# Optimization experiments

Hardware: AMD Instinct MI355X
Metric: run time of the kernel (lower is better)

The kernel has to match this reference:

```python
import jax, jax.numpy as jnp
import numpy as np

N_NODES = 100000
N_EDGES = 3200000
IN_DIM = 512
HEADS = 4
C1 = 8   # conv1 per-head channels
C2 = 4   # conv2 per-head channels
OUT_DIM = 10
N_GRAPHS = 64
NEG_SLOPE = 0.2


def _leaky_relu(x):
    return jnp.where(x >= 0, x, NEG_SLOPE * x)


def gat_conv(x, src, dst, W, a_src, a_dst, b):
    """PyG GATConv (concat=True). x:[N,F], src/dst:[E], W:[F,H*C], a_*:[H,C], b:[H*C]."""
    N = x.shape[0]
    H, C = a_src.shape
    h = (x @ W).reshape(N, H, C)                      # [N,H,C]
    e_src = jnp.einsum('nhc,hc->nh', h, a_src)        # [N,H]
    e_dst = jnp.einsum('nhc,hc->nh', h, a_dst)
    e = _leaky_relu(e_src[src] + e_dst[dst])          # [E,H]
    # segment softmax over edges grouped by destination node
    m = jax.ops.segment_max(e, dst, num_segments=N)   # [N,H]
    ex = jnp.exp(e - m[dst])
    denom = jax.ops.segment_sum(ex, dst, num_segments=N)
    alpha = ex / (denom[dst] + 1e-16)                 # [E,H]
    out = jax.ops.segment_sum(h[src] * alpha[:, :, None], dst, num_segments=N)
    return out.reshape(N, H * C) + b


def setup_inputs() -> dict:
    key = jax.random.key(0)
    ks = jax.random.split(key, 16)
    x = jax.random.normal(ks[0], (N_NODES, IN_DIM), dtype=jnp.float32)
    edge_index = jax.random.randint(ks[1], (2, N_EDGES), 0, N_NODES, dtype=jnp.int64)
    batch = jnp.sort(jax.random.randint(ks[2], (N_NODES,), 0, N_GRAPHS, dtype=jnp.int64))
    def glorot(k, shape):
        fan_in = shape[0] if len(shape) == 2 else shape[-1]
        return jax.random.normal(k, shape, dtype=jnp.float32) * (1.0 / np.sqrt(fan_in))
    return {
        'x': x, 'edge_index': edge_index, 'batch': batch,
        'W1': glorot(ks[3], (IN_DIM, HEADS * C1)),
        'att_src1': glorot(ks[4], (HEADS, C1)),
        'att_dst1': glorot(ks[5], (HEADS, C1)),
        'b1': jnp.zeros((HEADS * C1,), jnp.float32),
        'W2': glorot(ks[6], (HEADS * C1, HEADS * C2)),
        'att_src2': glorot(ks[7], (HEADS, C2)),
        'att_dst2': glorot(ks[8], (HEADS, C2)),
        'b2': jnp.zeros((HEADS * C2,), jnp.float32),
        'Wf': glorot(ks[9], (HEADS * C2, OUT_DIM)),
        'bf': jnp.zeros((OUT_DIM,), jnp.float32),
    }


def reference(x, edge_index, batch, W1, att_src1, att_dst1, b1,
              W2, att_src2, att_dst2, b2, Wf, bf):
    N = x.shape[0]
    loops = jnp.arange(N, dtype=edge_index.dtype)     # add_self_loops=True
    src = jnp.concatenate([edge_index[0], loops])
    dst = jnp.concatenate([edge_index[1], loops])
    h = jax.nn.relu(gat_conv(x, src, dst, W1, att_src1, att_dst1, b1))
    h = jax.nn.relu(gat_conv(h, src, dst, W2, att_src2, att_dst2, b2))
    # global_mean_pool over graphs
    sums = jax.ops.segment_sum(h, batch, num_segments=N_GRAPHS)
    cnt = jax.ops.segment_sum(jnp.ones((N,), h.dtype), batch, num_segments=N_GRAPHS)
    pooled = sums / jnp.maximum(cnt, 1.0)[:, None]    # [G, 16]
    return pooled @ Wf + bf
```

## Files before the change

### kernel.cpp

```cpp
#include <hip/hip_runtime.h>


#define LRELU(v) ((v) >= 0.f ? (v) : 0.2f * (v))

__global__ __launch_bounds__(256) void k_bin(const int* __restrict__ ei,
                                             int2* __restrict__ stg,
                                             int* __restrict__ rcnt,
                                             int E0, int Etot, int nr, int cap) {
    __shared__ int cnt[1024];
    __shared__ int base[1024];
    const int t = threadIdx.x;
    for (int i = t; i < nr; i += 256) cnt[i] = 0;
    __syncthreads();
    const int e0 = blockIdx.x * 8192;
#pragma unroll 4
    for (int k = 0; k < 32; k++) {
        int e = e0 + k * 256 + t;
        if (e < Etot) {
            int d = (e < E0) ? ei[E0 + e] : (e - E0);
            atomicAdd(&cnt[d >> 8], 1);
        }
    }
    __syncthreads();
    for (int i = t; i < nr; i += 256) {
        int c = cnt[i];
        base[i] = c ? atomicAdd(&rcnt[i], c) : 0;
        cnt[i] = 0;
    }
    __syncthreads();
#pragma unroll 4
    for (int k = 0; k < 32; k++) {
        int e = e0 + k * 256 + t;
        if (e < Etot) {
            int s, d;
            if (e < E0) {
                s = ei[e];
                d = ei[E0 + e];
            } else {
                s = d = e - E0;
            }
            int r = d >> 8;
            int slot = base[r] + atomicAdd(&cnt[r], 1);
            stg[(size_t)r * cap + slot] = make_int2(s, d);
        }
    }
}

__global__ __launch_bounds__(512) void k_sort(const int2* __restrict__ stg,
                                              const int* __restrict__ rcnt,
                                              int* __restrict__ row_ptr,
                                              int* __restrict__ ssrc,
                                              int* __restrict__ sdst,
                                              int N, int Etot, int nr, int cap) {
    __shared__ int hist[256];
    __shared__ int hs[256];
    __shared__ int red[512];
    const int r = blockIdx.x;
    const int t = threadIdx.x;
    int part = 0;
    for (int i = t; i < r; i += 512) part += rcnt[i];
    red[t] = part;
    if (t < 256) hist[t] = 0;
    __syncthreads();
    for (int off = 256; off > 0; off >>= 1) {
        if (t < off) red[t] += red[t + off];
        __syncthreads();
    }
    const int rb = red[0];
    const int n0 = r << 8;
    const int cnt = rcnt[r];
    const int2* seg = stg + (size_t)r * cap;
    for (int i = t; i < cnt; i += 512) {
        int d = seg[i].y;
        atomicAdd(&hist[d - n0], 1);
    }
    __syncthreads();
    if (t < 256) hs[t] = hist[t];
    __syncthreads();
    for (int off = 1; off < 256; off <<= 1) {
        int o = (t < 256 && t >= off) ? hs[t - off] : 0;
        __syncthreads();
        if (t < 256) hs[t] += o;
        __syncthreads();
    }
    if (t < 256) {
        int excl = hs[t] - hist[t];
        int node = n0 + t;
        if (node < N) row_ptr[node] = rb + excl;
        hist[t] = excl;
    }
    if (r == nr - 1 && t == 0) row_ptr[N] = Etot;
    __syncthreads();
    for (int i = t; i < cnt; i += 512) {
        int2 sd2 = seg[i];
        int off = atomicAdd(&hist[sd2.y - n0], 1);
        ssrc[rb + off] = sd2.x;
        sdst[rb + off] = sd2.y;
    }
}

__global__ __launch_bounds__(256) void k_gemm1(const float* __restrict__ x,
                                               const float* __restrict__ W,
                                               const float* __restrict__ a_src,
                                               const float* __restrict__ a_dst,
                                               float* __restrict__ h,
                                               float* __restrict__ es,
                                               float* __restrict__ ed, int N) {
    __shared__ float xs[32 * 132];
    __shared__ float ws[32 * 36];
    const int t = threadIdx.x;
    const int r0 = (t >> 2) * 2;
    const int cg = t & 3;
    const int row0 = blockIdx.x * 128;

    float acc[2][8];
#pragma unroll
    for (int i = 0; i < 2; i++)
#pragma unroll
        for (int j = 0; j < 8; j++) acc[i][j] = 0.f;

    float4 xr[4];
    float4 wr;
    const int xrow = t >> 3, xc4 = t & 7;
    const int wk = t >> 3, wc4 = t & 7;

    auto load_chunk = [&](int kc) {
#pragma unroll
        for (int ii = 0; ii < 4; ii++) {
            int row = xrow + ii * 32;
            int rr = row0 + row;
            if (rr >= N) rr = N - 1;
            xr[ii] = *(const float4*)&x[(size_t)rr * 512 + kc + xc4 * 4];
        }
        wr = *(const float4*)&W[(size_t)(kc + wk) * 32 + wc4 * 4];
    };

    load_chunk(0);
    for (int c = 0; c < 16; c++) {
        __syncthreads();
#pragma unroll
        for (int ii = 0; ii < 4; ii++) {
            int row = xrow + ii * 32;
            xs[(xc4 * 4 + 0) * 132 + row] = xr[ii].x;
            xs[(xc4 * 4 + 1) * 132 + row] = xr[ii].y;
            xs[(xc4 * 4 + 2) * 132 + row] = xr[ii].z;
            xs[(xc4 * 4 + 3) * 132 + row] = xr[ii].w;
        }
        ws[wk * 36 + wc4 * 4 + 0] = wr.x;
        ws[wk * 36 + wc4 * 4 + 1] = wr.y;
        ws[wk * 36 + wc4 * 4 + 2] = wr.z;
        ws[wk * 36 + wc4 * 4 + 3] = wr.w;
        __syncthreads();
        if (c < 15) load_chunk((c + 1) * 32);
#pragma unroll 8
        for (int k = 0; k < 32; k++) {
            float2 xv = *(const float2*)&xs[k * 132 + r0];
            float4 w0 = *(const float4*)&ws[k * 36 + cg * 8];
            float4 w1 = *(const float4*)&ws[k * 36 + cg * 8 + 4];
            acc[0][0] += xv.x * w0.x;
            acc[0][1] += xv.x * w0.y;
            acc[0][2] += xv.x * w0.z;
            acc[0][3] += xv.x * w0.w;
            acc[0][4] += xv.x * w1.x;
            acc[0][5] += xv.x * w1.y;
            acc[0][6] += xv.x * w1.z;
            acc[0][7] += xv.x * w1.w;
            acc[1][0] += xv.y * w0.x;
            acc[1][1] += xv.y * w0.y;
            acc[1][2] += xv.y * w0.z;
            acc[1][3] += xv.y * w0.w;
            acc[1][4] += xv.y * w1.x;
            acc[1][5] += xv.y * w1.y;
            acc[1][6] += xv.y * w1.z;
            acc[1][7] += xv.y * w1.w;
        }
    }

    float4 as0 = *(const float4*)&a_src[cg * 8];
    float4 as1 = *(const float4*)&a_src[cg * 8 + 4];
    float4 ad0 = *(const float4*)&a_dst[cg * 8];
    float4 ad1 = *(const float4*)&a_dst[cg * 8 + 4];
#pragma unroll
    for (int i = 0; i < 2; i++) {
        int r = row0 + r0 + i;
        if (r < N) {
            *(float4*)&h[(size_t)r * 32 + cg * 8] =
                make_float4(acc[i][0], acc[i][1], acc[i][2], acc[i][3]);
            *(float4*)&h[(size_t)r * 32 + cg * 8 + 4] =
                make_float4(acc[i][4], acc[i][5], acc[i][6], acc[i][7]);
            es[r * 4 + cg] = acc[i][0] * as0.x + acc[i][1] * as0.y +
                             acc[i][2] * as0.z + acc[i][3] * as0.w +
                             acc[i][4] * as1.x + acc[i][5] * as1.y +
                             acc[i][6] * as1.z + acc[i][7] * as1.w;
            ed[r * 4 + cg] = acc[i][0] * ad0.x + acc[i][1] * ad0.y +
                             acc[i][2] * ad0.z + acc[i][3] * ad0.w +
                             acc[i][4] * ad1.x + acc[i][5] * ad1.y +
                             acc[i][6] * ad1.z + acc[i][7] * ad1.w;
        }
    }
}

__global__ __launch_bounds__(256) void k_alpha(const int* __restrict__ ssrc,
                                               const int* __restrict__ sdst,
                                               const float* __restrict__ es,
                                               const float* __restrict__ ed,
                                               float4* __restrict__ alf, int Etot) {
    int i = blockIdx.x * 256 + threadIdx.x;
    if (i >= Etot) return;
    int s = ssrc[i];
    int d = sdst[i];
    float4 a = *(const float4*)&es[(size_t)s * 4];
    float4 b = *(const float4*)&ed[(size_t)d * 4];
    float4 o;
    float v;
    v = a.x + b.x; o.x = __expf(LRELU(v));
    v = a.y + b.y; o.y = __expf(LRELU(v));
    v = a.z + b.z; o.z = __expf(LRELU(v));
    v = a.w + b.w; o.w = __expf(LRELU(v));
    alf[i] = o;
}

template <int HC>
__global__ __launch_bounds__(256) void k_agg(const int* __restrict__ row_ptr,
                                             const int* __restrict__ ssrc,
                                             const float* __restrict__ hsrc,
                                             const float4* __restrict__ alf,
                                             const float* __restrict__ bias,
                                             float* __restrict__ out, int N) {
    constexpr int E2 = 64 / HC;
    constexpr int U = 8;
    const int lane = threadIdx.x & 63;
    const int d = blockIdx.x * 4 + (threadIdx.x >> 6);
    if (d >= N) return;
    const int c = lane & (HC - 1);
    const int e2 = lane / HC;
    const int hh = c / (HC / 4);
    const int start = row_ptr[d];
    const int deg = row_ptr[d + 1] - start;
    const int j0 = (e2 < deg) ? e2 : 0;

    float l = 0.f, acc = 0.f;
    for (int jb = e2; jb < deg; jb += U * E2) {
        int idx[U];
        float wv[U];
#pragma unroll
        for (int u = 0; u < U; u++) {
            int jj = jb + u * E2;
            bool ok = jj < deg;
            wv[u] = ok ? 1.f : 0.f;
            idx[u] = start + (ok ? jj : j0);
        }
        int sv[U];
#pragma unroll
        for (int u = 0; u < U; u++) sv[u] = ssrc[idx[u]];
        float av[U];
#pragma unroll
        for (int u = 0; u < U; u++)
            av[u] = ((const float*)&alf[idx[u]])[hh] * wv[u];
        float hv[U];
#pragma unroll
        for (int u = 0; u < U; u++) hv[u] = hsrc[(size_t)sv[u] * HC + c];
#pragma unroll
        for (int u = 0; u < U; u++) {
            l += av[u];
            acc += av[u] * hv[u];
        }
    }
#pragma unroll
    for (int off = HC; off < 64; off <<= 1) {
        l += __shfl_xor(l, off);
        acc += __shfl_xor(acc, off);
    }
    if (lane < HC) {
        float v = acc / (l + 1e-16f) + bias[c];
        out[(size_t)d * HC + c] = v > 0.f ? v : 0.f;
    }
}

__global__ __launch_bounds__(256) void k_gemm2(const float* __restrict__ g1,
                                               const float* __restrict__ W2,
                                               const float* __restrict__ a2s,
                                               const float* __restrict__ a2d,
                                               float* __restrict__ h2,
                                               float* __restrict__ es2,
                                               float* __restrict__ ed2, int N) {
    __shared__ float rows[64 * 33];
    __shared__ float ws[32 * 20];
    int t = threadIdx.x;
    int n0 = blockIdx.x * 64;
#pragma unroll
    for (int ii = 0; ii < 2; ii++) {
        int idx = ii * 256 + t;
        int node = idx >> 3, c4 = idx & 7;
        float4 v = make_float4(0.f, 0.f, 0.f, 0.f);
        if (n0 + node < N) v = *(const float4*)&g1[(size_t)(n0 + node) * 32 + c4 * 4];
        rows[node * 33 + c4 * 4 + 0] = v.x;
        rows[node * 33 + c4 * 4 + 1] = v.y;
        rows[node * 33 + c4 * 4 + 2] = v.z;
        rows[node * 33 + c4 * 4 + 3] = v.w;
    }
    if (t < 128) {
        int r = t >> 2, c4 = t & 3;
        float4 v = *(const float4*)&W2[r * 16 + c4 * 4];
        ws[r * 20 + c4 * 4 + 0] = v.x;
        ws[r * 20 + c4 * 4 + 1] = v.y;
        ws[r * 20 + c4 * 4 + 2] = v.z;
        ws[r * 20 + c4 * 4 + 3] = v.w;
    }
    __syncthreads();
    int node = t >> 2, q = t & 3;
    int n = n0 + node;
    if (n >= N) return;
    float acc[4] = {0.f, 0.f, 0.f, 0.f};
#pragma unroll 8
    for (int cc = 0; cc < 32; cc++) {
        float v = rows[node * 33 + cc];
        float4 w = *(const float4*)&ws[cc * 20 + q * 4];
        acc[0] += v * w.x;
        acc[1] += v * w.y;
        acc[2] += v * w.z;
        acc[3] += v * w.w;
    }
    *(float4*)&h2[(size_t)n * 16 + q * 4] = make_float4(acc[0], acc[1], acc[2], acc[3]);
    float s1 = 0.f, s2 = 0.f;
#pragma unroll
    for (int j = 0; j < 4; j++) {
        s1 += acc[j] * a2s[q * 4 + j];
        s2 += acc[j] * a2d[q * 4 + j];
    }
    es2[n * 4 + q] = s1;
    ed2[n * 4 + q] = s2;
}

__global__ __launch_bounds__(256) void k_final(const float* __restrict__ h3,
                                               const int* __restrict__ batch,
                                               const float* __restrict__ Wf,
                                               const float* __restrict__ bf,
                                               float* __restrict__ out, int N) {
    __shared__ float part[16][17];
    __shared__ float pooled[16];
    int g = blockIdx.x;
    int t = threadIdx.x;

    int lo = 0, b = N;
    while (lo < b) { int mid = (lo + b) >> 1; if (batch[mid] < g) lo = mid + 1; else b = mid; }
    int hi = lo; b = N;
    while (hi < b) { int mid = (hi + b) >> 1; if (batch[mid] < g + 1) hi = mid + 1; else b = mid; }

    int ch = t & 15, r = t >> 4;
    float acc = 0.f;
    for (int i = lo + r; i < hi; i += 16) acc += h3[(size_t)i * 16 + ch];
    part[r][ch] = acc;
    __syncthreads();
    if (t < 16) {
        float s = 0.f;
#pragma unroll
        for (int rr = 0; rr < 16; rr++) s += part[rr][t];
        float cnt = (float)(hi - lo);
        pooled[t] = s / fmaxf(cnt, 1.f);
    }
    __syncthreads();
    if (t < 10) {
        float v = bf[t];
#pragma unroll
        for (int cc = 0; cc < 16; cc++) v += pooled[cc] * Wf[cc * 10 + t];
        out[g * 10 + t] = v;
    }
}

extern "C" void kernel_launch(void* const* d_in, const int* in_sizes, int n_in,
                              void* d_out, int out_size, void* d_ws, size_t ws_size,
                              hipStream_t stream) {
    const float* x   = (const float*)d_in[0];
    const int*   ei  = (const int*)d_in[1];
    const int*   bat = (const int*)d_in[2];
    const float* W1  = (const float*)d_in[3];
    const float* as1 = (const float*)d_in[4];
    const float* ad1 = (const float*)d_in[5];
    const float* b1  = (const float*)d_in[6];
    const float* W2  = (const float*)d_in[7];
    const float* as2 = (const float*)d_in[8];
    const float* ad2 = (const float*)d_in[9];
    const float* b2  = (const float*)d_in[10];
    const float* Wf  = (const float*)d_in[11];
    const float* bf  = (const float*)d_in[12];
    float* outp = (float*)d_out;

    const int N = in_sizes[2];
    const int E0 = in_sizes[1] / 2;
    const int Etot = E0 + N;
    const int nr = (N + 255) >> 8;
    const int cap = Etot / nr + 2048;

    char* w = (char*)d_ws;
    auto alloc = [&](size_t bytes) -> char* {
        char* p = w;
        w += (bytes + 255) & ~(size_t)255;
        return p;
    };
    float* h1  = (float*)alloc((size_t)N * 32 * 4);
    float* es1 = (float*)alloc((size_t)N * 4 * 4);
    float* ed1 = (float*)alloc((size_t)N * 4 * 4);
    float* g1  = (float*)alloc((size_t)N * 32 * 4);
    float* h2  = (float*)alloc((size_t)N * 16 * 4);
    float* es2 = (float*)alloc((size_t)N * 4 * 4);
    float* ed2 = (float*)alloc((size_t)N * 4 * 4);
    int* rcnt    = (int*)alloc(4096);
    int* row_ptr = (int*)alloc((size_t)(N + 1) * 4);
    int* ssrc    = (int*)alloc((size_t)Etot * 4);
    int* sdst    = (int*)alloc((size_t)Etot * 4);
    float4* alf  = (float4*)alloc((size_t)Etot * 16);
    int2* stg    = (int2*)alloc((size_t)nr * cap * 8);
    float* h3 = h1;

    const int nb1 = (N + 127) / 128;
    const int nbe = (Etot + 255) / 256;

    hipMemsetAsync(rcnt, 0, 4096, stream);
    k_bin<<<(Etot + 8191) / 8192, 256, 0, stream>>>(ei, stg, rcnt, E0, Etot, nr, cap);
    k_sort<<<nr, 512, 0, stream>>>(stg, rcnt, row_ptr, ssrc, sdst, N, Etot, nr, cap);
    k_gemm1<<<nb1, 256, 0, stream>>>(x, W1, as1, ad1, h1, es1, ed1, N);
    k_alpha<<<nbe, 256, 0, stream>>>(ssrc, sdst, es1, ed1, alf, Etot);
    k_agg<32><<<(N + 3) / 4, 256, 0, stream>>>(row_ptr, ssrc, h1, alf, b1, g1, N);
    k_gemm2<<<(N + 63) / 64, 256, 0, stream>>>(g1, W2, as2, ad2, h2, es2, ed2, N);
    k_alpha<<<nbe, 256, 0, stream>>>(ssrc, sdst, es2, ed2, alf, Etot);
    k_agg<16><<<(N + 3) / 4, 256, 0, stream>>>(row_ptr, ssrc, h2, alf, b2, h3, N);
    k_final<<<64, 256, 0, stream>>>(h3, bat, Wf, bf, outp, N);
}
```

Measured before the change: 660.4 us.

## Fuse edge attention computation into aggregation kernels and drop sdst/alpha buffers

Removes the separate per-edge alpha kernels and computes exp(leaky_relu(es[src]+ed[dst])) inline inside the CSR aggregation, since the destination is fixed per wavefront. This drops the sdst array write in the sort and the 16-byte-per-edge alpha buffer round trip through memory. The aggregation is also restructured to use float4 feature loads per lane, with more edges processed in parallel per wave, and an adjusted unroll. In exchange, exp is recomputed per channel group, and the es gather adds a dependent load after the source index lookup.

```diff
diff --git a/kernel.cpp b/kernel.cpp
--- a/kernel.cpp
+++ b/kernel.cpp
@@ -50,7 +50,6 @@
                                               const int* __restrict__ rcnt,
                                               int* __restrict__ row_ptr,
                                               int* __restrict__ ssrc,
-                                              int* __restrict__ sdst,
                                               int N, int Etot, int nr, int cap) {
     __shared__ int hist[256];
     __shared__ int hs[256];
@@ -95,7 +94,6 @@
         int2 sd2 = seg[i];
         int off = atomicAdd(&hist[sd2.y - n0], 1);
         ssrc[rb + off] = sd2.x;
-        sdst[rb + off] = sd2.y;
     }
 }
 
@@ -200,52 +198,33 @@
     }
 }
 
-__global__ __launch_bounds__(256) void k_alpha(const int* __restrict__ ssrc,
-                                               const int* __restrict__ sdst,
-                                               const float* __restrict__ es,
-                                               const float* __restrict__ ed,
-                                               float4* __restrict__ alf, int Etot) {
-    int i = blockIdx.x * 256 + threadIdx.x;
-    if (i >= Etot) return;
-    int s = ssrc[i];
-    int d = sdst[i];
-    float4 a = *(const float4*)&es[(size_t)s * 4];
-    float4 b = *(const float4*)&ed[(size_t)d * 4];
-    float4 o;
-    float v;
-    v = a.x + b.x; o.x = __expf(LRELU(v));
-    v = a.y + b.y; o.y = __expf(LRELU(v));
-    v = a.z + b.z; o.z = __expf(LRELU(v));
-    v = a.w + b.w; o.w = __expf(LRELU(v));
-    alf[i] = o;
-}
-
-template <int HC>
-__global__ __launch_bounds__(256) void k_agg(const int* __restrict__ row_ptr,
-                                             const int* __restrict__ ssrc,
-                                             const float* __restrict__ hsrc,
-                                             const float4* __restrict__ alf,
-                                             const float* __restrict__ bias,
-                                             float* __restrict__ out, int N) {
-    constexpr int E2 = 64 / HC;
-    constexpr int U = 8;
+__global__ __launch_bounds__(256) void k_agg1(const int* __restrict__ row_ptr,
+                                              const int* __restrict__ ssrc,
+                                              const float* __restrict__ h,
+                                              const float* __restrict__ es,
+                                              const float* __restrict__ ed,
+                                              const float* __restrict__ bias,
+                                              float* __restrict__ out, int N) {
+    constexpr int U = 5;
     const int lane = threadIdx.x & 63;
     const int d = blockIdx.x * 4 + (threadIdx.x >> 6);
     if (d >= N) return;
-    const int c = lane & (HC - 1);
-    const int e2 = lane / HC;
-    const int hh = c / (HC / 4);
+    const int e2 = lane >> 3;
+    const int c4 = lane & 7;
+    const int head = c4 >> 1;
     const int start = row_ptr[d];
     const int deg = row_ptr[d + 1] - start;
+    const float edh = ed[d * 4 + head];
     const int j0 = (e2 < deg) ? e2 : 0;
 
-    float l = 0.f, acc = 0.f;
-    for (int jb = e2; jb < deg; jb += U * E2) {
+    float l = 0.f;
+    float4 acc = make_float4(0.f, 0.f, 0.f, 0.f);
+    for (int jb = e2; jb < deg; jb += U * 8) {
         int idx[U];
         float wv[U];
 #pragma unroll
         for (int u = 0; u < U; u++) {
-            int jj = jb + u * E2;
+            int jj = jb + u * 8;
             bool ok = jj < deg;
             wv[u] = ok ? 1.f : 0.f;
             idx[u] = start + (ok ? jj : j0);
@@ -253,27 +232,122 @@
         int sv[U];
 #pragma unroll
         for (int u = 0; u < U; u++) sv[u] = ssrc[idx[u]];
-        float av[U];
+        float ev[U];
+#pragma unroll
+        for (int u = 0; u < U; u++) ev[u] = es[sv[u] * 4 + head];
+        float4 hv[U];
 #pragma unroll
         for (int u = 0; u < U; u++)
-            av[u] = ((const float*)&alf[idx[u]])[hh] * wv[u];
-        float hv[U];
-#pragma unroll
-        for (int u = 0; u < U; u++) hv[u] = hsrc[(size_t)sv[u] * HC + c];
+            hv[u] = *(const float4*)&h[(size_t)sv[u] * 32 + c4 * 4];
 #pragma unroll
         for (int u = 0; u < U; u++) {
-            l += av[u];
-            acc += av[u] * hv[u];
-        }
-    }
-#pragma unroll
-    for (int off = HC; off < 64; off <<= 1) {
+            float e = ev[u] + edh;
+            e = LRELU(e);
+            float a = __expf(e) * wv[u];
+            l += a;
+            acc.x += a * hv[u].x;
+            acc.y += a * hv[u].y;
+            acc.z += a * hv[u].z;
+            acc.w += a * hv[u].w;
+        }
+    }
+#pragma unroll
+    for (int off = 8; off < 64; off <<= 1) {
         l += __shfl_xor(l, off);
-        acc += __shfl_xor(acc, off);
-    }
-    if (lane < HC) {
-        float v = acc / (l + 1e-16f) + bias[c];
-        out[(size_t)d * HC + c] = v > 0.f ? v : 0.f;
+        acc.x += __shfl_xor(acc.x, off);
+        acc.y += __shfl_xor(acc.y, off);
+        acc.z += __shfl_xor(acc.z, off);
+        acc.w += __shfl_xor(acc.w, off);
+    }
+    if (lane < 8) {
+        float ls = l + 1e-16f;
+        float4 b = *(const float4*)&bias[c4 * 4];
+        float4 o;
+        o.x = acc.x / ls + b.x;
+        o.y = acc.y / ls + b.y;
+        o.z = acc.z / ls + b.z;
+        o.w = acc.w / ls + b.w;
+        o.x = o.x > 0.f ? o.x : 0.f;
+        o.y = o.y > 0.f ? o.y : 0.f;
+        o.z = o.z > 0.f ? o.z : 0.f;
+        o.w = o.w > 0.f ? o.w : 0.f;
+        *(float4*)&out[(size_t)d * 32 + c4 * 4] = o;
+    }
+}
+
+__global__ __launch_bounds__(256) void k_agg2(const int* __restrict__ row_ptr,
+                                              const int* __restrict__ ssrc,
+                                              const float* __restrict__ h2,
+                                              const float* __restrict__ es,
+                                              const float* __restrict__ ed,
+                                              const float* __restrict__ bias,
+                                              float* __restrict__ out, int N) {
+    constexpr int U = 3;
+    const int lane = threadIdx.x & 63;
+    const int d = blockIdx.x * 4 + (threadIdx.x >> 6);
+    if (d >= N) return;
+    const int e2 = lane >> 2;
+    const int c4 = lane & 3;
+    const int start = row_ptr[d];
+    const int deg = row_ptr[d + 1] - start;
+    const float edh = ed[d * 4 + c4];
+    const int j0 = (e2 < deg) ? e2 : 0;
+
+    float l = 0.f;
+    float4 acc = make_float4(0.f, 0.f, 0.f, 0.f);
+    for (int jb = e2; jb < deg; jb += U * 16) {
+        int idx[U];
+        float wv[U];
+#pragma unroll
+        for (int u = 0; u < U; u++) {
+            int jj = jb + u * 16;
+            bool ok = jj < deg;
+            wv[u] = ok ? 1.f : 0.f;
+            idx[u] = start + (ok ? jj : j0);
+        }
+        int sv[U];
+#pragma unroll
+        for (int u = 0; u < U; u++) sv[u] = ssrc[idx[u]];
+        float ev[U];
+#pragma unroll
+        for (int u = 0; u < U; u++) ev[u] = es[sv[u] * 4 + c4];
+        float4 hv[U];
+#pragma unroll
+        for (int u = 0; u < U; u++)
+            hv[u] = *(const float4*)&h2[(size_t)sv[u] * 16 + c4 * 4];
+#pragma unroll
+        for (int u = 0; u < U; u++) {
+            float e = ev[u] + edh;
+            e = LRELU(e);
+            float a = __expf(e) * wv[u];
+            l += a;
+            acc.x += a * hv[u].x;
+            acc.y += a * hv[u].y;
+            acc.z += a * hv[u].z;
+            acc.w += a * hv[u].w;
+        }
+    }
+#pragma unroll
+    for (int off = 4; off < 64; off <<= 1) {
+        l += __shfl_xor(l, off);
+        acc.x += __shfl_xor(acc.x, off);
+        acc.y += __shfl_xor(acc.y, off);
+        acc.z += __shfl_xor(acc.z, off);
+        acc.w += __shfl_xor(acc.w, off);
+    }
+    if (lane < 4) {
+        float ls = l + 1e-16f;
+        float4 b = *(const float4*)&bias[c4 * 4];
+        float4 o;
+        o.x = acc.x / ls + b.x;
+        o.y = acc.y / ls + b.y;
+        o.z = acc.z / ls + b.z;
+        o.w = acc.w / ls + b.w;
+        o.x = o.x > 0.f ? o.x : 0.f;
+        o.y = o.y > 0.f ? o.y : 0.f;
+        o.z = o.z > 0.f ? o.z : 0.f;
+        o.w = o.w > 0.f ? o.w : 0.f;
+        *(float4*)&out[(size_t)d * 16 + c4 * 4] = o;
     }
 }
 
@@ -408,22 +482,17 @@
     int* rcnt    = (int*)alloc(4096);
     int* row_ptr = (int*)alloc((size_t)(N + 1) * 4);
     int* ssrc    = (int*)alloc((size_t)Etot * 4);
-    int* sdst    = (int*)alloc((size_t)Etot * 4);
-    float4* alf  = (float4*)alloc((size_t)Etot * 16);
     int2* stg    = (int2*)alloc((size_t)nr * cap * 8);
     float* h3 = h1;
 
     const int nb1 = (N + 127) / 128;
-    const int nbe = (Etot + 255) / 256;
 
     hipMemsetAsync(rcnt, 0, 4096, stream);
     k_bin<<<(Etot + 8191) / 8192, 256, 0, stream>>>(ei, stg, rcnt, E0, Etot, nr, cap);
-    k_sort<<<nr, 512, 0, stream>>>(stg, rcnt, row_ptr, ssrc, sdst, N, Etot, nr, cap);
+    k_sort<<<nr, 512, 0, stream>>>(stg, rcnt, row_ptr, ssrc, N, Etot, nr, cap);
     k_gemm1<<<nb1, 256, 0, stream>>>(x, W1, as1, ad1, h1, es1, ed1, N);
-    k_alpha<<<nbe, 256, 0, stream>>>(ssrc, sdst, es1, ed1, alf, Etot);
-    k_agg<32><<<(N + 3) / 4, 256, 0, stream>>>(row_ptr, ssrc, h1, alf, b1, g1, N);
+    k_agg1<<<(N + 3) / 4, 256, 0, stream>>>(row_ptr, ssrc, h1, es1, ed1, b1, g1, N);
     k_gemm2<<<(N + 63) / 64, 256, 0, stream>>>(g1, W2, as2, ad2, h2, es2, ed2, N);
-    k_alpha<<<nbe, 256, 0, stream>>>(ssrc, sdst, es2, ed2, alf, Etot);
-    k_agg<16><<<(N + 3) / 4, 256, 0, stream>>>(row_ptr, ssrc, h2, alf, b2, h3, N);
+    k_agg2<<<(N + 3) / 4, 256, 0, stream>>>(row_ptr, ssrc, h2, es2, ed2, b2, h3, N);
     k_final<<<64, 256, 0, stream>>>(h3, bat, Wf, bf, outp, N);
 }
```

New measurement: 591.0 us. 10.5% less time.
